# Kernel optimization log

Measured on AMD Instinct MI355X. Metric: run time of the kernel, lower is better.

Reference implementation:

```python
import jax, jax.numpy as jnp
import numpy as np

B, S, H = 1, 2048, 4096
NH, NKV, HD = 32, 8, 128
N_REP = NH // NKV
SCALING = HD ** -0.5
ROPE_THETA = 10000.0
NEG_INF = -1e9


def setup_inputs() -> dict:
    key = jax.random.key(0)
    ks = jax.random.split(key, 5)
    hidden_states = jax.random.normal(ks[0], (B, S, H), dtype=jnp.float32)
    # torch nn.Linear weights are [out_features, in_features]
    wq = jax.random.normal(ks[1], (NH * HD, H), dtype=jnp.float32) * 0.02
    wk = jax.random.normal(ks[2], (NKV * HD, H), dtype=jnp.float32) * 0.02
    wv = jax.random.normal(ks[3], (NKV * HD, H), dtype=jnp.float32) * 0.02
    wo = jax.random.normal(ks[4], (NH * HD, H), dtype=jnp.float32).T * 0.02  # [H, NH*HD] -> store as [out,in]=[H,4096]
    wo = jnp.asarray(wo)
    # RoPE tables: [1, S, HD]
    inv_freq = 1.0 / (ROPE_THETA ** (jnp.arange(0, HD, 2, dtype=jnp.float32) / HD))
    pos = jnp.arange(S, dtype=jnp.float32)
    freqs = pos[:, None] * inv_freq[None, :]            # [S, HD/2]
    emb = jnp.concatenate([freqs, freqs], axis=-1)      # [S, HD]
    cos = jnp.cos(emb)[None]
    sin = jnp.sin(emb)[None]
    # additive causal mask [1, 1, S, S]
    causal = jnp.tril(jnp.ones((S, S), dtype=bool))
    attn_mask = jnp.where(causal, 0.0, NEG_INF).astype(jnp.float32)[None, None]
    return {"hidden_states": hidden_states, "wq": wq, "wk": wk, "wv": wv,
            "wo": wo, "cos": cos, "sin": sin, "attn_mask": attn_mask}


def rotate_half(x):
    x1, x2 = jnp.split(x, 2, axis=-1)
    return jnp.concatenate([-x2, x1], axis=-1)


def reference(hidden_states, wq, wk, wv, wo, cos, sin, attn_mask):
    b, s, _ = hidden_states.shape
    # projections (x @ W.T), reshape to [B, heads, S, HD]
    q = (hidden_states @ wq.T).reshape(b, s, NH, HD).transpose(0, 2, 1, 3)
    k = (hidden_states @ wk.T).reshape(b, s, NKV, HD).transpose(0, 2, 1, 3)
    v = (hidden_states @ wv.T).reshape(b, s, NKV, HD).transpose(0, 2, 1, 3)
    # RoPE (unsqueeze_dim=1)
    c = cos[:, None]  # [1,1,S,HD]
    sn = sin[:, None]
    q = q * c + rotate_half(q) * sn
    k = k * c + rotate_half(k) * sn
    # GQA head repeat
    k = jnp.repeat(k, N_REP, axis=1)  # [B, NH, S, HD]
    v = jnp.repeat(v, N_REP, axis=1)
    # eager attention
    scores = jnp.einsum('bhqd,bhkd->bhqk', q, k) * SCALING + attn_mask[:, :, :, :s]
    attn_weights = jax.nn.softmax(scores.astype(jnp.float32), axis=-1).astype(q.dtype)
    attn_out = jnp.einsum('bhqk,bhkd->bhqd', attn_weights, v)
    attn_out = attn_out.transpose(0, 2, 1, 3).reshape(b, s, NH * HD)
    out = attn_out @ wo.T
    return out, attn_weights
```

## Files before the change

kernel.cpp:

```cpp
#include <hip/hip_runtime.h>
#include <cstdint>
#include <cstddef>


#define SEQ 2048
#define HID 4096
#define NH_ 32
#define NKV_ 8
#define HD_ 128
#define KDIM_KV 1024
#define SCALING 0.08838834764831843f

typedef __bf16 bf16;
typedef __attribute__((ext_vector_type(8))) __bf16 bf16x8;
typedef __attribute__((ext_vector_type(4))) float f32x4;

__device__ __forceinline__ unsigned short f2bf(float f) {
  __bf16 h = (__bf16)f;
  return __builtin_bit_cast(unsigned short, h);
}
__device__ __forceinline__ float bf2f(unsigned short u) {
  unsigned int x = ((unsigned int)u) << 16;
  return __builtin_bit_cast(float, x);
}

__device__ __forceinline__ void async16(const void* g, void* l) {
  __builtin_amdgcn_global_load_lds(
      (const __attribute__((address_space(1))) unsigned int*)g,
      (__attribute__((address_space(3))) unsigned int*)l, 16, 0, 0);
}

__global__ __launch_bounds__(256) void cvt_kernel(const float* __restrict__ src,
                                                  bf16* __restrict__ dst, int n4) {
  int i = blockIdx.x * 256 + threadIdx.x;
  if (i >= n4) return;
  float4 v = ((const float4*)src)[i];
  union { unsigned short u[4]; uint2 vv; } pk;
  pk.u[0] = f2bf(v.x); pk.u[1] = f2bf(v.y);
  pk.u[2] = f2bf(v.z); pk.u[3] = f2bf(v.w);
  ((uint2*)dst)[i] = pk.vv;
}

template <int AR>
__device__ __forceinline__ void gemm256_loop(const char* __restrict__ Ab,
                                             const char* __restrict__ Bb,
                                             char* smem,
                                             f32x4 (&acc)[AR * 4][4]) {
  const int NT = 128;
  const int tid = threadIdx.x;
  const int wid = tid >> 6, lane = tid & 63;
  const int quad = lane >> 4, l16 = lane & 15;
  const int wm = wid >> 2, wn = wid & 3;
  const int ASZ = AR * 8192;
  const int SLOT = ASZ + 16384;

  const char* gA0 = Ab + (size_t)(tid >> 2) * 8192 + (size_t)(tid & 3) * 16;
  const char* gA1 = gA0 + (size_t)128 * 8192;
  const char* gB0 = Bb + (size_t)(tid >> 2) * 8192 + (size_t)(tid & 3) * 16;
  const char* gB1 = gB0 + (size_t)128 * 8192;
  const int ldsA0 = wid * 1024;
  const int ldsB0 = ASZ + wid * 1024;

  const f32x4 fz = {0.f, 0.f, 0.f, 0.f};
#pragma unroll
  for (int m = 0; m < AR * 4; m++)
#pragma unroll
    for (int n = 0; n < 4; n++) acc[m][n] = fz;

#pragma unroll
  for (int t = 0; t < 2; t++) {
    char* sl = smem + t * SLOT;
    async16(gA0 + t * 64, sl + ldsA0);
    if (AR == 2) async16(gA1 + t * 64, sl + ldsA0 + 8192);
    async16(gB0 + t * 64, sl + ldsB0);
    async16(gB1 + t * 64, sl + ldsB0 + 8192);
  }

#pragma unroll 3
  for (int t = 0; t < NT; t++) {
    if (t + 1 < NT) {
      if (AR == 2) asm volatile("s_waitcnt vmcnt(4)" ::: "memory");
      else         asm volatile("s_waitcnt vmcnt(3)" ::: "memory");
    } else {
      asm volatile("s_waitcnt vmcnt(0)" ::: "memory");
    }
    __builtin_amdgcn_s_barrier();
    __builtin_amdgcn_sched_barrier(0);
    if (t + 2 < NT) {
      char* sl = smem + ((t + 2) % 3) * SLOT;
      async16(gA0 + (size_t)(t + 2) * 64, sl + ldsA0);
      if (AR == 2) async16(gA1 + (size_t)(t + 2) * 64, sl + ldsA0 + 8192);
    }
    const bf16* sA = (const bf16*)(smem + (t % 3) * SLOT);
    const bf16* sB = (const bf16*)(smem + (t % 3) * SLOT + ASZ);
    bf16x8 a[AR * 2], b[4];
#pragma unroll
    for (int m = 0; m < AR * 2; m++)
      a[m] = *(const bf16x8*)(sA + (size_t)(wm * (AR * 64) + m * 16 + l16) * 32 + quad * 8);
#pragma unroll
    for (int n = 0; n < 4; n++)
      b[n] = *(const bf16x8*)(sB + (size_t)(wn * 64 + n * 16 + l16) * 32 + quad * 8);
    __builtin_amdgcn_s_setprio(1);
#pragma unroll
    for (int m = 0; m < AR * 2; m++)
#pragma unroll
      for (int n = 0; n < 4; n++)
        acc[m][n] = __builtin_amdgcn_mfma_f32_16x16x32_bf16(a[m], b[n], acc[m][n], 0, 0, 0);
    __builtin_amdgcn_s_setprio(0);
    __builtin_amdgcn_s_barrier();
    __builtin_amdgcn_sched_barrier(0);
    if (t + 2 < NT) {
      char* sl = smem + ((t + 2) % 3) * SLOT;
      async16(gB0 + (size_t)(t + 2) * 64, sl + ldsB0);
      async16(gB1 + (size_t)(t + 2) * 64, sl + ldsB0 + 8192);
    }
#pragma unroll
    for (int m = 0; m < AR * 2; m++)
      a[m] = *(const bf16x8*)(sA + (size_t)(wm * (AR * 64) + (AR * 2 + m) * 16 + l16) * 32 + quad * 8);
    __builtin_amdgcn_s_setprio(1);
#pragma unroll
    for (int m = 0; m < AR * 2; m++)
#pragma unroll
      for (int n = 0; n < 4; n++)
        acc[AR * 2 + m][n] =
            __builtin_amdgcn_mfma_f32_16x16x32_bf16(a[m], b[n], acc[AR * 2 + m][n], 0, 0, 0);
    __builtin_amdgcn_s_setprio(0);
  }
}

__global__ __launch_bounds__(512, 2) void qkv_gemm(
    const bf16* __restrict__ A,
    const bf16* __restrict__ Wq,
    const bf16* __restrict__ Wk,
    const bf16* __restrict__ Wv,
    const float* __restrict__ cosp,
    const float* __restrict__ sinp,
    bf16* __restrict__ qout,
    bf16* __restrict__ kout,
    bf16* __restrict__ vtout)
{
  extern __shared__ char smem[];
  const int mi = blockIdx.x, nt = blockIdx.y;
  const int tid = threadIdx.x;
  const int wid = tid >> 6, lane = tid & 63;
  const int quad = lane >> 4, l16 = lane & 15;
  const int wm = wid >> 2, wn = wid & 3;

  const bf16* Bp;
  if (nt < 16)      Bp = Wq + (size_t)nt * 256 * HID;
  else if (nt < 20) Bp = Wk + (size_t)(nt - 16) * 256 * HID;
  else              Bp = Wv + (size_t)(nt - 20) * 256 * HID;

  f32x4 acc[8][4];
  gemm256_loop<2>((const char*)(A + (size_t)mi * 256 * HID), (const char*)Bp,
                  smem, acc);

  __syncthreads();
  float* ct = (float*)smem;
  for (int ch = 0; ch < 4; ch++) {
    if (wm == (ch >> 1)) {
#pragma unroll
      for (int mm = 0; mm < 4; mm++)
#pragma unroll
        for (int n = 0; n < 4; n++)
#pragma unroll
          for (int r = 0; r < 4; r++)
            ct[(size_t)(mm * 16 + quad * 4 + r) * 265 + wn * 64 + n * 16 + l16] =
                acc[(ch & 1) * 4 + mm][n][r];
    }
    __syncthreads();
    if (nt < 20) {
      const int r0 = tid >> 5, c8 = (tid & 31) << 3;
      bf16* outp; int ldo, colbase;
      if (nt < 16) { outp = qout; ldo = HID; colbase = nt * 256; }
      else         { outp = kout; ldo = KDIM_KV; colbase = (nt - 16) * 256; }
      const int d0 = c8 & 127;
      const bool lo = d0 < 64;
#pragma unroll
      for (int p = 0; p < 4; p++) {
        int row = p * 16 + r0;
        int s = mi * 256 + ch * 64 + row;
        union { unsigned short u[8]; uint4 v; } pk;
#pragma unroll
        for (int u8 = 0; u8 < 8; u8++) {
          int c = c8 + u8;
          float x  = ct[(size_t)row * 265 + c];
          float xp = ct[(size_t)row * 265 + (c ^ 64)];
          float cv = cosp[(size_t)s * HD_ + d0 + u8];
          float sv = sinp[(size_t)s * HD_ + d0 + u8];
          pk.u[u8] = f2bf(lo ? x * cv - xp * sv : x * cv + xp * sv);
        }
        *(uint4*)(outp + (size_t)s * ldo + colbase + c8) = pk.v;
      }
    } else {
      const int dcol = tid & 255, sb = (tid >> 8) << 3;
      const int vh = (nt - 20) * 2 + (dcol >> 7), dd = dcol & 127;
#pragma unroll
      for (int i = 0; i < 4; i++) {
        int s8 = sb + i * 16;
        union { unsigned short u[8]; uint4 v; } pk;
#pragma unroll
        for (int u8 = 0; u8 < 8; u8++)
          pk.u[u8] = f2bf(ct[(size_t)(s8 + u8) * 265 + dcol]);
        *(uint4*)(vtout + ((size_t)vh * HD_ + dd) * SEQ + mi * 256 + ch * 64 + s8) = pk.v;
      }
    }
    __syncthreads();
  }
}

__device__ __forceinline__ void stage128(const bf16* __restrict__ base, int row_stride,
                                         unsigned short (*buf)[136], int tid) {
  const int r0 = tid >> 4;
  const int c = (tid & 15) * 8;
#pragma unroll
  for (int g = 0; g < 8; g++) {
    int row = g * 16 + r0;
    uint4 v = *(const uint4*)(base + (size_t)row * row_stride + c);
    *(uint4*)&buf[row][c] = v;
  }
}

__global__ __launch_bounds__(256, 3) void attn_kernel(
    const bf16* __restrict__ qb,
    const bf16* __restrict__ kb,
    const bf16* __restrict__ vtb,
    float* __restrict__ wout,
    bf16* __restrict__ aout)
{
  const int bid = blockIdx.x;
  const int h = bid & 31;
  const int qt = 31 - (bid >> 5);
  const int kvh = h >> 2;
  const int tid = threadIdx.x;
  const int wave = tid >> 6, lane = tid & 63;
  const int quad = lane >> 4, l16 = lane & 15;
  const int kmax = qt >> 1;

  __shared__ __align__(16) unsigned short kvbuf[128][136];
  __shared__ __align__(16) unsigned short wlds[64][136];

  {
    const int kc0 = (kmax + 1) * 128;
    if (kc0 < SEQ) {
      const float4 z = make_float4(0.f, 0.f, 0.f, 0.f);
      for (int row = 0; row < 64; row++) {
        float* zrow = wout + ((size_t)h * SEQ + (size_t)qt * 64 + row) * SEQ;
        for (int c = kc0 + (tid << 2); c < SEQ; c += 1024)
          *(float4*)(zrow + c) = z;
      }
    }
  }

  bf16x8 aq[4];
  {
    const bf16* qbase = qb + ((size_t)(qt * 64) + wave * 16 + l16) * HID + h * HD_;
#pragma unroll
    for (int ks = 0; ks < 4; ks++)
      aq[ks] = *(const bf16x8*)(qbase + ks * 32 + quad * 8);
  }

  float m_[4], l_[4];
#pragma unroll
  for (int r = 0; r < 4; r++) { m_[r] = -3.0e38f; l_[r] = 0.f; }

  for (int kt = 0; kt <= kmax; kt++) {
    __syncthreads();
    stage128(kb + (size_t)(kt * 128) * KDIM_KV + kvh * HD_, KDIM_KV, kvbuf, tid);
    __syncthreads();

    f32x4 acc[8];
    const f32x4 fz = {0.f, 0.f, 0.f, 0.f};
#pragma unroll
    for (int j = 0; j < 8; j++) acc[j] = fz;
#pragma unroll
    for (int ks = 0; ks < 4; ks++) {
      bf16x8 bk[8];
#pragma unroll
      for (int j = 0; j < 8; j++)
        bk[j] = *(const bf16x8*)&kvbuf[j * 16 + l16][ks * 32 + quad * 8];
#pragma unroll
      for (int j = 0; j < 8; j++)
        acc[j] = __builtin_amdgcn_mfma_f32_16x16x32_bf16(aq[ks], bk[j], acc[j], 0, 0, 0);
    }

    const bool mc = (kt == kmax);
#pragma unroll
    for (int r = 0; r < 4; r++) {
      int qrow = qt * 64 + wave * 16 + quad * 4 + r;
      float sv[8], mx = -3.0e38f;
#pragma unroll
      for (int j = 0; j < 8; j++) {
        float s = acc[j][r] * SCALING;
        if (mc && (kt * 128 + j * 16 + l16) > qrow) s -= 1.0e9f;
        sv[j] = s;
        mx = fmaxf(mx, s);
      }
#pragma unroll
      for (int sh = 1; sh < 16; sh <<= 1) mx = fmaxf(mx, __shfl_xor(mx, sh));
      float mn = fmaxf(m_[r], mx);
      float sum = 0.f;
#pragma unroll
      for (int j = 0; j < 8; j++) sum += __expf(sv[j] - mn);
#pragma unroll
      for (int sh = 1; sh < 16; sh <<= 1) sum += __shfl_xor(sum, sh);
      l_[r] = l_[r] * __expf(m_[r] - mn) + sum;
      m_[r] = mn;
    }
  }

  float linv[4];
#pragma unroll
  for (int r = 0; r < 4; r++) linv[r] = 1.f / l_[r];

  f32x4 oac[8];
  {
    const f32x4 fz = {0.f, 0.f, 0.f, 0.f};
#pragma unroll
    for (int j = 0; j < 8; j++) oac[j] = fz;
  }

  for (int kt = 0; kt <= kmax; kt++) {
    __syncthreads();
    stage128(kb + (size_t)(kt * 128) * KDIM_KV + kvh * HD_, KDIM_KV, kvbuf, tid);
    __syncthreads();

    f32x4 acc[8];
    const f32x4 fz = {0.f, 0.f, 0.f, 0.f};
#pragma unroll
    for (int j = 0; j < 8; j++) acc[j] = fz;
#pragma unroll
    for (int ks = 0; ks < 4; ks++) {
      bf16x8 bk[8];
#pragma unroll
      for (int j = 0; j < 8; j++)
        bk[j] = *(const bf16x8*)&kvbuf[j * 16 + l16][ks * 32 + quad * 8];
#pragma unroll
      for (int j = 0; j < 8; j++)
        acc[j] = __builtin_amdgcn_mfma_f32_16x16x32_bf16(aq[ks], bk[j], acc[j], 0, 0, 0);
    }

    const bool mc = (kt == kmax);
#pragma unroll
    for (int r = 0; r < 4; r++) {
      int qrow = qt * 64 + wave * 16 + quad * 4 + r;
#pragma unroll
      for (int j = 0; j < 8; j++) {
        float s = acc[j][r] * SCALING;
        if (mc && (kt * 128 + j * 16 + l16) > qrow) s -= 1.0e9f;
        wlds[wave * 16 + quad * 4 + r][j * 16 + l16] = f2bf(__expf(s - m_[r]) * linv[r]);
      }
    }
    __syncthreads();

    stage128(vtb + (size_t)kvh * HD_ * SEQ + kt * 128, SEQ, kvbuf, tid);
    {
      float* wdst = wout + ((size_t)h * SEQ + (size_t)qt * 64) * SEQ + kt * 128;
      const int rr = tid >> 5, c4 = (tid & 31) << 2;
#pragma unroll
      for (int p = 0; p < 8; p++) {
        int row = p * 8 + rr;
        uint2 w = *(const uint2*)&wlds[row][c4];
        float4 v;
        v.x = bf2f((unsigned short)(w.x & 0xffff));
        v.y = bf2f((unsigned short)(w.x >> 16));
        v.z = bf2f((unsigned short)(w.y & 0xffff));
        v.w = bf2f((unsigned short)(w.y >> 16));
        *(float4*)(wdst + (size_t)row * SEQ + c4) = v;
      }
    }
    __syncthreads();

#pragma unroll
    for (int ks = 0; ks < 4; ks++) {
      bf16x8 aw, bv[8];
      aw = *(const bf16x8*)&wlds[wave * 16 + l16][ks * 32 + quad * 8];
#pragma unroll
      for (int j = 0; j < 8; j++)
        bv[j] = *(const bf16x8*)&kvbuf[j * 16 + l16][ks * 32 + quad * 8];
#pragma unroll
      for (int j = 0; j < 8; j++)
        oac[j] = __builtin_amdgcn_mfma_f32_16x16x32_bf16(aw, bv[j], oac[j], 0, 0, 0);
    }
  }

  __syncthreads();
#pragma unroll
  for (int j = 0; j < 8; j++)
#pragma unroll
    for (int r = 0; r < 4; r++)
      wlds[wave * 16 + quad * 4 + r][j * 16 + l16] = f2bf(oac[j][r]);
  __syncthreads();
  {
    const int r0 = tid >> 4, c8 = (tid & 15) << 3;
    bf16* abase = aout + (size_t)(qt * 64) * HID + h * HD_;
#pragma unroll
    for (int p = 0; p < 4; p++) {
      int row = p * 16 + r0;
      union { unsigned short u[8]; uint4 v; } pk;
#pragma unroll
      for (int u8 = 0; u8 < 8; u8++) pk.u[u8] = wlds[row][c8 + u8];
      *(uint4*)(abase + (size_t)row * HID + c8) = pk.v;
    }
  }
}

__global__ __launch_bounds__(512, 2) void proj_gemm(const bf16* __restrict__ A,
                                                    const bf16* __restrict__ B,
                                                    float* __restrict__ C) {
  extern __shared__ char smem[];
  const int mi = blockIdx.x, nt = blockIdx.y;
  const int tid = threadIdx.x;
  const int lane = tid & 63;
  const int wid = tid >> 6;
  const int quad = lane >> 4, l16 = lane & 15;
  const int wm = wid >> 2, wn = wid & 3;

  f32x4 acc[4][4];
  gemm256_loop<1>((const char*)(A + (size_t)mi * 128 * HID),
                  (const char*)(B + (size_t)nt * 256 * HID), smem, acc);

#pragma unroll
  for (int m = 0; m < 4; m++)
#pragma unroll
    for (int n = 0; n < 4; n++)
#pragma unroll
      for (int r = 0; r < 4; r++) {
        int row = mi * 128 + wm * 64 + m * 16 + quad * 4 + r;
        int col = nt * 256 + wn * 64 + n * 16 + l16;
        C[(size_t)row * HID + col] = acc[m][n][r];
      }
}

extern "C" void kernel_launch(void* const* d_in, const int* in_sizes, int n_in,
                              void* d_out, int out_size, void* d_ws, size_t ws_size,
                              hipStream_t stream) {
  const float* hs   = (const float*)d_in[0];
  const float* wq   = (const float*)d_in[1];
  const float* wk   = (const float*)d_in[2];
  const float* wv   = (const float*)d_in[3];
  const float* wo   = (const float*)d_in[4];
  const float* cosp = (const float*)d_in[5];
  const float* sinp = (const float*)d_in[6];

  if (ws_size < (size_t)109051904) return;

  char* ws = (char*)d_ws;
  bf16* hsb = (bf16*)(ws + 0);
  bf16* wqb = (bf16*)(ws + 16777216);
  bf16* wkb = (bf16*)(ws + 50331648);
  bf16* wvb = (bf16*)(ws + 58720256);
  bf16* qb  = (bf16*)(ws + 67108864);
  bf16* kb  = (bf16*)(ws + 83886080);
  bf16* vtb = (bf16*)(ws + 88080384);
  bf16* aob = (bf16*)(ws + 92274688);

  float* outp = (float*)d_out;
  float* wout = outp + (size_t)SEQ * HID;

  hipFuncSetAttribute((const void*)qkv_gemm,
                      hipFuncAttributeMaxDynamicSharedMemorySize, 98304);
  hipFuncSetAttribute((const void*)proj_gemm,
                      hipFuncAttributeMaxDynamicSharedMemorySize, 73728);

  cvt_kernel<<<2097152 / 256, 256, 0, stream>>>(hs, hsb, 2097152);
  cvt_kernel<<<4194304 / 256, 256, 0, stream>>>(wq, wqb, 4194304);
  cvt_kernel<<<1048576 / 256, 256, 0, stream>>>(wk, wkb, 1048576);
  cvt_kernel<<<1048576 / 256, 256, 0, stream>>>(wv, wvb, 1048576);

  qkv_gemm<<<dim3(8, 24), 512, 98304, stream>>>(hsb, wqb, wkb, wvb, cosp, sinp, qb, kb, vtb);

  cvt_kernel<<<4194304 / 256, 256, 0, stream>>>(wo, wqb, 4194304);

  attn_kernel<<<1024, 256, 0, stream>>>(qb, kb, vtb, wout, aob);

  proj_gemm<<<dim3(16, 16), 512, 73728, stream>>>(aob, wqb, outp);
}
```

Before: 1.037 ms.

## Double attention query tile to 128 rows per block to halve K/V restaging

Each attention block now processes 128 query rows (two 16-row groups per wave) instead of 64, so every staged K and V tile feeds twice as many MFMAs. The grid shrinks from 1024 to 512 blocks, and the second pass splits score computation into two halves to limit register pressure. This cuts the redundant global-to-LDS loads of K and V, at the cost of more registers, a larger LDS footprint, lower occupancy (launch bounds 3 to 2 blocks) and fewer blocks to balance the causal workload.

```diff
diff --git a/kernel.cpp b/kernel.cpp
--- a/kernel.cpp
+++ b/kernel.cpp
@@ -221,7 +221,7 @@
   }
 }
 
-__global__ __launch_bounds__(256, 3) void attn_kernel(
+__global__ __launch_bounds__(256, 2) void attn_kernel(
     const bf16* __restrict__ qb,
     const bf16* __restrict__ kb,
     const bf16* __restrict__ vtb,
@@ -230,49 +230,54 @@
 {
   const int bid = blockIdx.x;
   const int h = bid & 31;
-  const int qt = 31 - (bid >> 5);
+  const int qt = 15 - (bid >> 5);
   const int kvh = h >> 2;
   const int tid = threadIdx.x;
   const int wave = tid >> 6, lane = tid & 63;
   const int quad = lane >> 4, l16 = lane & 15;
-  const int kmax = qt >> 1;
+  const int kmax = qt;
 
   __shared__ __align__(16) unsigned short kvbuf[128][136];
-  __shared__ __align__(16) unsigned short wlds[64][136];
+  __shared__ __align__(16) unsigned short wlds[128][136];
 
   {
     const int kc0 = (kmax + 1) * 128;
     if (kc0 < SEQ) {
       const float4 z = make_float4(0.f, 0.f, 0.f, 0.f);
-      for (int row = 0; row < 64; row++) {
-        float* zrow = wout + ((size_t)h * SEQ + (size_t)qt * 64 + row) * SEQ;
+      for (int row = 0; row < 128; row++) {
+        float* zrow = wout + ((size_t)h * SEQ + (size_t)qt * 128 + row) * SEQ;
         for (int c = kc0 + (tid << 2); c < SEQ; c += 1024)
           *(float4*)(zrow + c) = z;
       }
     }
   }
 
-  bf16x8 aq[4];
-  {
-    const bf16* qbase = qb + ((size_t)(qt * 64) + wave * 16 + l16) * HID + h * HD_;
+  bf16x8 aq[2][4];
+#pragma unroll
+  for (int g = 0; g < 2; g++) {
+    const bf16* qbase = qb + ((size_t)(qt * 128) + wave * 32 + g * 16 + l16) * HID + h * HD_;
 #pragma unroll
     for (int ks = 0; ks < 4; ks++)
-      aq[ks] = *(const bf16x8*)(qbase + ks * 32 + quad * 8);
-  }
-
-  float m_[4], l_[4];
-#pragma unroll
-  for (int r = 0; r < 4; r++) { m_[r] = -3.0e38f; l_[r] = 0.f; }
+      aq[g][ks] = *(const bf16x8*)(qbase + ks * 32 + quad * 8);
+  }
+
+  float m_[2][4], l_[2][4];
+#pragma unroll
+  for (int g = 0; g < 2; g++)
+#pragma unroll
+    for (int r = 0; r < 4; r++) { m_[g][r] = -3.0e38f; l_[g][r] = 0.f; }
 
   for (int kt = 0; kt <= kmax; kt++) {
     __syncthreads();
     stage128(kb + (size_t)(kt * 128) * KDIM_KV + kvh * HD_, KDIM_KV, kvbuf, tid);
     __syncthreads();
 
-    f32x4 acc[8];
+    f32x4 acc[2][8];
     const f32x4 fz = {0.f, 0.f, 0.f, 0.f};
 #pragma unroll
-    for (int j = 0; j < 8; j++) acc[j] = fz;
+    for (int g = 0; g < 2; g++)
+#pragma unroll
+      for (int j = 0; j < 8; j++) acc[g][j] = fz;
 #pragma unroll
     for (int ks = 0; ks < 4; ks++) {
       bf16x8 bk[8];
@@ -280,44 +285,52 @@
       for (int j = 0; j < 8; j++)
         bk[j] = *(const bf16x8*)&kvbuf[j * 16 + l16][ks * 32 + quad * 8];
 #pragma unroll
-      for (int j = 0; j < 8; j++)
-        acc[j] = __builtin_amdgcn_mfma_f32_16x16x32_bf16(aq[ks], bk[j], acc[j], 0, 0, 0);
+      for (int g = 0; g < 2; g++)
+#pragma unroll
+        for (int j = 0; j < 8; j++)
+          acc[g][j] = __builtin_amdgcn_mfma_f32_16x16x32_bf16(aq[g][ks], bk[j], acc[g][j], 0, 0, 0);
     }
 
     const bool mc = (kt == kmax);
 #pragma unroll
-    for (int r = 0; r < 4; r++) {
-      int qrow = qt * 64 + wave * 16 + quad * 4 + r;
-      float sv[8], mx = -3.0e38f;
-#pragma unroll
-      for (int j = 0; j < 8; j++) {
-        float s = acc[j][r] * SCALING;
-        if (mc && (kt * 128 + j * 16 + l16) > qrow) s -= 1.0e9f;
-        sv[j] = s;
-        mx = fmaxf(mx, s);
-      }
-#pragma unroll
-      for (int sh = 1; sh < 16; sh <<= 1) mx = fmaxf(mx, __shfl_xor(mx, sh));
-      float mn = fmaxf(m_[r], mx);
-      float sum = 0.f;
-#pragma unroll
-      for (int j = 0; j < 8; j++) sum += __expf(sv[j] - mn);
-#pragma unroll
-      for (int sh = 1; sh < 16; sh <<= 1) sum += __shfl_xor(sum, sh);
-      l_[r] = l_[r] * __expf(m_[r] - mn) + sum;
-      m_[r] = mn;
-    }
-  }
-
-  float linv[4];
-#pragma unroll
-  for (int r = 0; r < 4; r++) linv[r] = 1.f / l_[r];
-
-  f32x4 oac[8];
+    for (int g = 0; g < 2; g++)
+#pragma unroll
+      for (int r = 0; r < 4; r++) {
+        int qrow = qt * 128 + wave * 32 + g * 16 + quad * 4 + r;
+        float sv[8], mx = -3.0e38f;
+#pragma unroll
+        for (int j = 0; j < 8; j++) {
+          float s = acc[g][j][r] * SCALING;
+          if (mc && (kt * 128 + j * 16 + l16) > qrow) s -= 1.0e9f;
+          sv[j] = s;
+          mx = fmaxf(mx, s);
+        }
+#pragma unroll
+        for (int sh = 1; sh < 16; sh <<= 1) mx = fmaxf(mx, __shfl_xor(mx, sh));
+        float mn = fmaxf(m_[g][r], mx);
+        float sum = 0.f;
+#pragma unroll
+        for (int j = 0; j < 8; j++) sum += __expf(sv[j] - mn);
+#pragma unroll
+        for (int sh = 1; sh < 16; sh <<= 1) sum += __shfl_xor(sum, sh);
+        l_[g][r] = l_[g][r] * __expf(m_[g][r] - mn) + sum;
+        m_[g][r] = mn;
+      }
+  }
+
+  float linv[2][4];
+#pragma unroll
+  for (int g = 0; g < 2; g++)
+#pragma unroll
+    for (int r = 0; r < 4; r++) linv[g][r] = 1.f / l_[g][r];
+
+  f32x4 oac[2][8];
   {
     const f32x4 fz = {0.f, 0.f, 0.f, 0.f};
 #pragma unroll
-    for (int j = 0; j < 8; j++) oac[j] = fz;
+    for (int g = 0; g < 2; g++)
+#pragma unroll
+      for (int j = 0; j < 8; j++) oac[g][j] = fz;
   }
 
   for (int kt = 0; kt <= kmax; kt++) {
@@ -325,40 +338,49 @@
     stage128(kb + (size_t)(kt * 128) * KDIM_KV + kvh * HD_, KDIM_KV, kvbuf, tid);
     __syncthreads();
 
-    f32x4 acc[8];
-    const f32x4 fz = {0.f, 0.f, 0.f, 0.f};
-#pragma unroll
-    for (int j = 0; j < 8; j++) acc[j] = fz;
-#pragma unroll
-    for (int ks = 0; ks < 4; ks++) {
-      bf16x8 bk[8];
-#pragma unroll
-      for (int j = 0; j < 8; j++)
-        bk[j] = *(const bf16x8*)&kvbuf[j * 16 + l16][ks * 32 + quad * 8];
-#pragma unroll
-      for (int j = 0; j < 8; j++)
-        acc[j] = __builtin_amdgcn_mfma_f32_16x16x32_bf16(aq[ks], bk[j], acc[j], 0, 0, 0);
-    }
-
     const bool mc = (kt == kmax);
 #pragma unroll
-    for (int r = 0; r < 4; r++) {
-      int qrow = qt * 64 + wave * 16 + quad * 4 + r;
-#pragma unroll
-      for (int j = 0; j < 8; j++) {
-        float s = acc[j][r] * SCALING;
-        if (mc && (kt * 128 + j * 16 + l16) > qrow) s -= 1.0e9f;
-        wlds[wave * 16 + quad * 4 + r][j * 16 + l16] = f2bf(__expf(s - m_[r]) * linv[r]);
-      }
+    for (int jh = 0; jh < 2; jh++) {
+      f32x4 acc[2][4];
+      const f32x4 fz = {0.f, 0.f, 0.f, 0.f};
+#pragma unroll
+      for (int g = 0; g < 2; g++)
+#pragma unroll
+        for (int j = 0; j < 4; j++) acc[g][j] = fz;
+#pragma unroll
+      for (int ks = 0; ks < 4; ks++) {
+        bf16x8 bk[4];
+#pragma unroll
+        for (int j = 0; j < 4; j++)
+          bk[j] = *(const bf16x8*)&kvbuf[(jh * 4 + j) * 16 + l16][ks * 32 + quad * 8];
+#pragma unroll
+        for (int g = 0; g < 2; g++)
+#pragma unroll
+          for (int j = 0; j < 4; j++)
+            acc[g][j] = __builtin_amdgcn_mfma_f32_16x16x32_bf16(aq[g][ks], bk[j], acc[g][j], 0, 0, 0);
+      }
+#pragma unroll
+      for (int g = 0; g < 2; g++)
+#pragma unroll
+        for (int r = 0; r < 4; r++) {
+          int qrow = qt * 128 + wave * 32 + g * 16 + quad * 4 + r;
+#pragma unroll
+          for (int j = 0; j < 4; j++) {
+            float s = acc[g][j][r] * SCALING;
+            if (mc && (kt * 128 + (jh * 4 + j) * 16 + l16) > qrow) s -= 1.0e9f;
+            wlds[wave * 32 + g * 16 + quad * 4 + r][(jh * 4 + j) * 16 + l16] =
+                f2bf(__expf(s - m_[g][r]) * linv[g][r]);
+          }
+        }
     }
     __syncthreads();
 
     stage128(vtb + (size_t)kvh * HD_ * SEQ + kt * 128, SEQ, kvbuf, tid);
     {
-      float* wdst = wout + ((size_t)h * SEQ + (size_t)qt * 64) * SEQ + kt * 128;
+      float* wdst = wout + ((size_t)h * SEQ + (size_t)qt * 128) * SEQ + kt * 128;
       const int rr = tid >> 5, c4 = (tid & 31) << 2;
 #pragma unroll
-      for (int p = 0; p < 8; p++) {
+      for (int p = 0; p < 16; p++) {
         int row = p * 8 + rr;
         uint2 w = *(const uint2*)&wlds[row][c4];
         float4 v;
@@ -373,29 +395,35 @@
 
 #pragma unroll
     for (int ks = 0; ks < 4; ks++) {
-      bf16x8 aw, bv[8];
-      aw = *(const bf16x8*)&wlds[wave * 16 + l16][ks * 32 + quad * 8];
+      bf16x8 aw0, aw1, bv[8];
+      aw0 = *(const bf16x8*)&wlds[wave * 32 + l16][ks * 32 + quad * 8];
+      aw1 = *(const bf16x8*)&wlds[wave * 32 + 16 + l16][ks * 32 + quad * 8];
 #pragma unroll
       for (int j = 0; j < 8; j++)
         bv[j] = *(const bf16x8*)&kvbuf[j * 16 + l16][ks * 32 + quad * 8];
 #pragma unroll
       for (int j = 0; j < 8; j++)
-        oac[j] = __builtin_amdgcn_mfma_f32_16x16x32_bf16(aw, bv[j], oac[j], 0, 0, 0);
+        oac[0][j] = __builtin_amdgcn_mfma_f32_16x16x32_bf16(aw0, bv[j], oac[0][j], 0, 0, 0);
+#pragma unroll
+      for (int j = 0; j < 8; j++)
+        oac[1][j] = __builtin_amdgcn_mfma_f32_16x16x32_bf16(aw1, bv[j], oac[1][j], 0, 0, 0);
     }
   }
 
   __syncthreads();
 #pragma unroll
-  for (int j = 0; j < 8; j++)
-#pragma unroll
-    for (int r = 0; r < 4; r++)
-      wlds[wave * 16 + quad * 4 + r][j * 16 + l16] = f2bf(oac[j][r]);
+  for (int g = 0; g < 2; g++)
+#pragma unroll
+    for (int j = 0; j < 8; j++)
+#pragma unroll
+      for (int r = 0; r < 4; r++)
+        wlds[wave * 32 + g * 16 + quad * 4 + r][j * 16 + l16] = f2bf(oac[g][j][r]);
   __syncthreads();
   {
     const int r0 = tid >> 4, c8 = (tid & 15) << 3;
-    bf16* abase = aout + (size_t)(qt * 64) * HID + h * HD_;
-#pragma unroll
-    for (int p = 0; p < 4; p++) {
+    bf16* abase = aout + (size_t)(qt * 128) * HID + h * HD_;
+#pragma unroll
+    for (int p = 0; p < 8; p++) {
       int row = p * 16 + r0;
       union { unsigned short u[8]; uint4 v; } pk;
 #pragma unroll
@@ -472,7 +500,7 @@
 
   cvt_kernel<<<4194304 / 256, 256, 0, stream>>>(wo, wqb, 4194304);
 
-  attn_kernel<<<1024, 256, 0, stream>>>(qb, kb, vtb, wout, aob);
+  attn_kernel<<<512, 256, 0, stream>>>(qb, kb, vtb, wout, aob);
 
   proj_gemm<<<dim3(16, 16), 512, 73728, stream>>>(aob, wqb, outp);
 }
```

Result: slower. 1.146 ms (+10.5%).
